# Performance work log

Hardware: AMD Instinct MI355X
Metric: run time of the kernel (lower is better)

## Reference

```python
import jax, jax.numpy as jnp
import numpy as np

MAX_RADIUS = 4.0
N_BASIS = 10
MUL = 8                    # output_size -> '8x0e' multiplicity
OUT_MULS = (16, 8, 4)      # irreps_output = 16x0e + 8x1o + 4x2e
L_DIMS = (1, 3, 5)
N_NODES = 10000
N_EDGES = 131072
N_GRAPHS = 64
WEIGHT_NUMEL = MUL * MUL * sum(OUT_MULS)  # 1792


def _silu(x):
    return x * jax.nn.sigmoid(x)


def _sph_harm(u):
    # e3nn real spherical harmonics lmax=2, normalize=True, 'component' normalization
    x, y, z = u[:, 0], u[:, 1], u[:, 2]
    s3, s5, s15 = 3.0 ** 0.5, 5.0 ** 0.5, 15.0 ** 0.5
    sh0 = jnp.ones_like(x)[:, None]
    sh1 = jnp.stack([s3 * x, s3 * y, s3 * z], -1)
    sh2 = jnp.stack([s15 * x * z, s15 * x * y,
                     s5 * (y * y - 0.5 * (x * x + z * z)),
                     s15 * y * z, 0.5 * s15 * (z * z - x * x)], -1)
    return sh0, sh1, sh2


def _soft_one_hot(x):
    # e3nn soft_one_hot_linspace, basis='gaussian', cutoff=True
    values = jnp.linspace(0.0, MAX_RADIUS, N_BASIS + 2)[1:-1]
    step = MAX_RADIUS / (N_BASIS + 1)
    diff = (x[:, None] - values) / step
    return jnp.exp(-diff * diff) / 1.12


def setup_inputs() -> dict:
    key = jax.random.key(0)
    ks = jax.random.split(key, 16)
    return {
        "pos": jax.random.normal(ks[0], (N_NODES, 3), jnp.float32) * 2.0,
        "A": jax.random.randint(ks[1], (N_NODES,), 0, 10),
        "batch": jnp.sort(jax.random.randint(ks[2], (N_NODES,), 0, N_GRAPHS)),
        "edge_src": jax.random.randint(ks[3], (N_EDGES,), 0, N_NODES),
        "edge_dst": jax.random.randint(ks[4], (N_EDGES,), 0, N_NODES),
        "edge_shifts": jax.random.normal(ks[5], (N_EDGES, 3), jnp.float32) * 0.1,
        "cell": jax.random.normal(ks[6], (N_GRAPHS, 3, 3), jnp.float32),
        "embed_table": jax.random.normal(ks[7], (10, 16), jnp.float32),
        "fit_W1": jax.random.normal(ks[8], (16, 64), jnp.float32) * (2.0 / 16) ** 0.5,
        "fit_b1": jnp.zeros((64,), jnp.float32),
        "fit_W2": jax.random.normal(ks[9], (64, 32), jnp.float32) * (2.0 / 64) ** 0.5,
        "fit_b2": jnp.zeros((32,), jnp.float32),
        "fit_W3": jax.random.normal(ks[10], (32, MUL), jnp.float32) * (2.0 / 32) ** 0.5,
        "fit_b3": jnp.zeros((MUL,), jnp.float32),
        "fc_W1": jax.random.normal(ks[11], (N_BASIS, 64), jnp.float32),
        "fc_W2": jax.random.normal(ks[12], (64, 64), jnp.float32),
        "fc_W3": jax.random.normal(ks[13], (64, 64), jnp.float32),
        "fc_W4": jax.random.normal(ks[14], (64, WEIGHT_NUMEL), jnp.float32),
    }


def reference(pos, A, batch, edge_src, edge_dst, edge_shifts, cell,
              embed_table, fit_W1, fit_b1, fit_W2, fit_b2, fit_W3, fit_b3,
              fc_W1, fc_W2, fc_W3, fc_W4):
    # --- edge vectors with periodic shifts ---
    shift_vecs = jnp.einsum('ni,nij->nj', edge_shifts, cell[batch[edge_src]])
    edge_vec = pos[edge_dst] - pos[edge_src] + shift_vecs      # [E,3]
    edge_length = jnp.linalg.norm(edge_vec, axis=1)            # [E]
    unit = edge_vec / jnp.maximum(edge_length, 1e-9)[:, None]

    # --- per-node scalar features: embedding -> MLP (MainNet2) ---
    h = embed_table[A]
    h = _silu(h @ fit_W1 + fit_b1)
    h = _silu(h @ fit_W2 + fit_b2)
    Ai = h @ fit_W3 + fit_b3                                   # [N,8]

    sh0, sh1, sh2 = _sph_harm(unit)                            # [E,1],[E,3],[E,5]

    # --- radial MLP (e3nn FullyConnectedNet: silu, 1/sqrt(fan_in) weight scaling) ---
    emb = _soft_one_hot(edge_length) * (N_BASIS ** 0.5)
    w = _silu(emb @ fc_W1 / N_BASIS ** 0.5)
    w = _silu(w @ fc_W2 / 8.0)
    w = _silu(w @ fc_W3 / 8.0)
    w = w @ fc_W4 / 8.0                                        # [E,1792]

    Ai_src = Ai[edge_src]                                      # [E,8]
    Ai_dst = Ai[edge_dst]                                      # [E,8]

    # FullTensorProduct(8x0e, sh) is the outer product f_in[e,u,m] = Ai_src[e,u]*sh_l[e,m];
    # FullyConnectedTensorProduct with scalar irreps_in2 reduces per l-channel to a
    # weighted contraction with path normalization 1/sqrt(mul1*mul2) = 1/8.
    blocks, off = [], 0
    for mul_out, dim, sh_l in zip(OUT_MULS, L_DIMS, (sh0, sh1, sh2)):
        n = MUL * MUL * mul_out
        Wl = w[:, off:off + n].reshape(-1, MUL, MUL, mul_out)
        off += n
        blk = jnp.einsum('eu,em,ev,euvw->ewm', Ai_src, sh_l, Ai_dst, Wl) / MUL
        blocks.append(blk.reshape(-1, mul_out * dim))
    edge_features = jnp.concatenate(blocks, -1)                # [E,60]

    # --- scatter-mean aggregation to destination nodes ---
    n_nodes = pos.shape[0]
    counts = jax.ops.segment_sum(jnp.ones((edge_dst.shape[0],), jnp.float32),
                                 edge_dst, num_segments=n_nodes)
    out = jax.ops.segment_sum(edge_features, edge_dst, num_segments=n_nodes)
    return out / jnp.maximum(counts, 1.0)[:, None]             # [N,60]
```

## Files before the change

kernel.cpp:

```cpp
#include <hip/hip_runtime.h>
#include <hip/hip_bf16.h>
#include <math.h>

#define NN 10000
#define NE 131072

typedef __attribute__((ext_vector_type(8))) short short8;
typedef __attribute__((ext_vector_type(4))) float f32x4;

__device__ __forceinline__ float silu_f(float x) {
    return x / (1.0f + __expf(-x));
}

__device__ __forceinline__ unsigned short f2bf(float f) {
    unsigned int u = __float_as_uint(f);
    u += 0x7FFFu + ((u >> 16) & 1u);
    return (unsigned short)(u >> 16);
}

__device__ __forceinline__ unsigned int pk_bf16(float lo, float hi) {
    __hip_bfloat162 h = __float22bfloat162_rn(float2{lo, hi});
    return *reinterpret_cast<unsigned int*>(&h);
}

__global__ __launch_bounds__(256)
void prep_kernel(const int* __restrict__ A,
                 const int* __restrict__ edst,
                 const float* __restrict__ emb_tab,
                 const float* __restrict__ W1, const float* __restrict__ b1,
                 const float* __restrict__ W2, const float* __restrict__ b2,
                 const float* __restrict__ W3, const float* __restrict__ b3,
                 const float* __restrict__ fcW1,
                 const float* __restrict__ fcW2,
                 const float* __restrict__ fcW3,
                 const float* __restrict__ fcW4,
                 int* __restrict__ hist,
                 int* __restrict__ rank,
                 float* __restrict__ outg,
                 float* __restrict__ Ai,
                 unsigned short* __restrict__ Wg,
                 unsigned short* __restrict__ Bg)
{
    const int blk = blockIdx.x;
    const int tid = threadIdx.x;

    if (blk < 40) {
        int nd = blk * 256 + tid;
        if (nd >= NN) return;
        int a = A[nd];
        float h[16];
#pragma unroll
        for (int i = 0; i < 16; ++i) h[i] = emb_tab[a * 16 + i];
        float h1[64];
#pragma unroll
        for (int j = 0; j < 64; ++j) h1[j] = b1[j];
#pragma unroll
        for (int i = 0; i < 16; ++i) {
            float hv = h[i];
#pragma unroll
            for (int j = 0; j < 64; ++j) h1[j] += hv * W1[i * 64 + j];
        }
#pragma unroll
        for (int j = 0; j < 64; ++j) h1[j] = silu_f(h1[j]);
        float h2[32];
#pragma unroll
        for (int j = 0; j < 32; ++j) h2[j] = b2[j];
#pragma unroll
        for (int i = 0; i < 64; ++i) {
            float hv = h1[i];
#pragma unroll
            for (int j = 0; j < 32; ++j) h2[j] += hv * W2[i * 32 + j];
        }
#pragma unroll
        for (int j = 0; j < 32; ++j) h2[j] = silu_f(h2[j]);
#pragma unroll
        for (int j = 0; j < 8; ++j) {
            float s = b3[j];
#pragma unroll
            for (int i = 0; i < 32; ++i) s += h2[i] * W3[i * 8 + j];
            Ai[nd * 8 + j] = s;
        }
    } else if (blk < 80) {
        int i = (blk - 40) * 256 + tid;
        int j    = i & 7;
        int lane = (i >> 3) & 63;
        int f    = i >> 9;
        int q = lane >> 4, n = lane & 15;
        int L, kf, nt;
        if (f < 4)       { L = 1; kf = 0;             nt = f; }
        else if (f < 12) { L = 2; kf = (f - 4) >> 2;  nt = (f - 4) & 3; }
        else             { L = 3; kf = (f - 12) >> 2; nt = (f - 12) & 3; }
        int k = kf * 32 + q * 8 + j;
        int col = nt * 16 + n;
        float v = 0.0f;
        if (L == 1)      { if (k < 10) v = fcW1[k * 64 + col]; }
        else if (L == 2) v = fcW2[k * 64 + col];
        else             v = fcW3[k * 64 + col];
        Wg[i] = f2bf(v);
    } else if (blk < 592) {
        int linear = (blk - 80) * 256 + tid;
        rank[linear] = atomicAdd(&hist[edst[linear]], 1);
        if (linear < 114688) {
            int k = linear / 1792;
            int t = linear - k * 1792;
            int uv, wc;
            if (t < 1024)      { uv = t >> 4;            wc = t & 15; }
            else if (t < 1536) { int r = t - 1024; uv = r >> 3; wc = 16 + (r & 7); }
            else               { int r = t - 1536; uv = r >> 2; wc = 24 + (r & 3); }
            int h  = uv >> 5;
            int q  = (uv >> 3) & 3;
            int j  = uv & 7;
            int nt = wc >> 4;
            int n  = wc & 15;
            int i  = (k << 11) | (h << 10) | (nt << 9) | (((q << 4) | n) << 3) | j;
            Bg[i] = f2bf(fcW4[linear]);
        } else {
            int z  = linear - 114688;
            int k  = z >> 8;
            int r  = z & 255;
            int uv = r >> 2;
            int c2 = z & 3;
            int h  = uv >> 5;
            int q  = (uv >> 3) & 3;
            int j  = uv & 7;
            int i  = (k << 11) | (h << 10) | (1 << 9) | (((q << 4) | (12 + c2)) << 3) | j;
            Bg[i] = 0;
        }
    } else {
        int t = (blk - 592) * 256 + tid;
        float4 z = float4{0.f, 0.f, 0.f, 0.f};
        for (int r = t; r < 150000; r += 25600)
            ((float4*)outg)[r] = z;
    }
}

__global__ __launch_bounds__(256)
void scanrank_kernel(const int* __restrict__ edst,
                     const int* __restrict__ hist,
                     const int* __restrict__ rank,
                     int* __restrict__ sortidx)
{
    __shared__ int offs[NN];
    __shared__ int part[256];
    const int tid = threadIdx.x;

    int loc[40];
    int s = 0;
    if (tid < 250) {
        const int4* h4 = (const int4*)(hist) + tid * 10;
#pragma unroll
        for (int v = 0; v < 10; ++v) {
            int4 x = h4[v];
            loc[v * 4 + 0] = x.x; loc[v * 4 + 1] = x.y;
            loc[v * 4 + 2] = x.z; loc[v * 4 + 3] = x.w;
            s += x.x + x.y + x.z + x.w;
        }
    } else {
#pragma unroll
        for (int r = 0; r < 40; ++r) loc[r] = 0;
    }
    part[tid] = s;
    __syncthreads();
#pragma unroll
    for (int off = 1; off < 256; off <<= 1) {
        int v = (tid >= off) ? part[tid - off] : 0;
        __syncthreads();
        part[tid] += v;
        __syncthreads();
    }
    if (tid < 250) {
        int run = part[tid] - s;
        int base = tid * 40;
#pragma unroll
        for (int r = 0; r < 40; ++r) { offs[base + r] = run; run += loc[r]; }
    }
    __syncthreads();

    int e = blockIdx.x * 256 + tid;
    int d = edst[e];
    sortidx[offs[d] + rank[e]] = e;
}

__global__ __launch_bounds__(256, 2)
void edge_fused_kernel(const float* __restrict__ pos,
                       const int* __restrict__ batch,
                       const int* __restrict__ esrc,
                       const int* __restrict__ edst,
                       const float* __restrict__ shifts,
                       const float* __restrict__ cell,
                       const unsigned short* __restrict__ Wg,
                       const unsigned short* __restrict__ Bg,
                       const int* __restrict__ sortidx,
                       const float* __restrict__ Ai,
                       const int* __restrict__ hist,
                       float* __restrict__ out_g)
{
    __shared__ __align__(16) unsigned short actb[4][64 * 68];
    __shared__ int   sdb[256];
    __shared__ __align__(16) float shb[4][64 * 8];

    const int tid  = threadIdx.x;
    const int wave = tid >> 6;
    const int lane = tid & 63;
    const int q    = lane >> 4;
    const int n    = lane & 15;
    const int i    = blockIdx.x * 256 + wave * 64 + lane;

    unsigned short* actw = actb[wave];

    int e = sortidx[i];
    int s = esrc[e], d = edst[e];
    sdb[wave * 64 + lane] = s | (d << 16);
    int b = batch[s];
    const float* C = cell + b * 9;
    float sx = shifts[e * 3 + 0], sy = shifts[e * 3 + 1], sz = shifts[e * 3 + 2];
    float vx = pos[d * 3 + 0] - pos[s * 3 + 0] + sx * C[0] + sy * C[3] + sz * C[6];
    float vy = pos[d * 3 + 1] - pos[s * 3 + 1] + sx * C[1] + sy * C[4] + sz * C[7];
    float vz = pos[d * 3 + 2] - pos[s * 3 + 2] + sx * C[2] + sy * C[5] + sz * C[8];
    float len = sqrtf(vx * vx + vy * vy + vz * vz);
    float inv = 1.0f / fmaxf(len, 1e-9f);
    float ux = vx * inv, uy = vy * inv, uz = vz * inv;
    {
        const float s3c  = 1.7320508075688772f;
        const float s5c  = 2.2360679774997896f;
        const float s15c = 3.872983346207417f;
        float* shw = shb[wave];
        *(float4*)&shw[lane * 8]     = float4{s3c * ux, s3c * uy, s3c * uz,
                                              s15c * ux * uz};
        *(float4*)&shw[lane * 8 + 4] = float4{s15c * ux * uy,
                                              s5c * (uy * uy - 0.5f * (ux * ux + uz * uz)),
                                              s15c * uy * uz,
                                              0.5f * s15c * (uz * uz - ux * ux)};
    }

    float embv[10];
    float base = len * 2.75f;
#pragma unroll
    for (int ii = 0; ii < 10; ++ii) {
        float ddv = base - (float)(ii + 1);
        embv[ii] = __expf(-ddv * ddv) * (1.0f / 1.12f);
    }
    {
        unsigned int u0 = pk_bf16(embv[0], embv[1]);
        unsigned int u1 = pk_bf16(embv[2], embv[3]);
        unsigned int u2 = pk_bf16(embv[4], embv[5]);
        unsigned int u3 = pk_bf16(embv[6], embv[7]);
        unsigned int u4 = pk_bf16(embv[8], embv[9]);
        uint2* arow = (uint2*)&actw[lane * 68];
        arow[0] = uint2{u0, u1};
        arow[1] = uint2{u2, u3};
        arow[2] = uint2{u4, 0u};
        arow[3] = uint2{0u, 0u};
        arow[4] = uint2{0u, 0u};
        arow[5] = uint2{0u, 0u};
        arow[6] = uint2{0u, 0u};
        arow[7] = uint2{0u, 0u};
    }

    union AF { unsigned int u[4]; short8 s8; };
    const f32x4 Z4 = (f32x4){0.f, 0.f, 0.f, 0.f};

    auto loadA = [&](int t, int kf) -> AF {
        const unsigned short* ap = &actw[(t * 16 + n) * 68 + kf * 32 + q * 8];
        uint2 a = *(const uint2*)ap;
        uint2 c = *(const uint2*)(ap + 4);
        AF f; f.u[0] = a.x; f.u[1] = a.y; f.u[2] = c.x; f.u[3] = c.y;
        return f;
    };
    auto loadW = [&](int f) -> short8 {
        return *(const short8*)&Wg[(f * 64 + lane) * 8];
    };

    {
        AF A1[4];
#pragma unroll
        for (int t = 0; t < 4; ++t) A1[t] = loadA(t, 0);
#pragma unroll
        for (int nt = 0; nt < 4; ++nt) {
            short8 W0 = loadW(nt);
            f32x4 Cc[4];
#pragma unroll
            for (int t = 0; t < 4; ++t)
                Cc[t] = __builtin_amdgcn_mfma_f32_16x16x32_bf16(A1[t].s8, W0, Z4, 0, 0, 0);
#pragma unroll
            for (int t = 0; t < 4; ++t)
#pragma unroll
                for (int r = 0; r < 4; ++r)
                    actw[(t * 16 + q * 4 + r) * 68 + nt * 16 + n] = f2bf(silu_f(Cc[t][r]));
        }
    }

    {
        AF A2[4][2];
#pragma unroll
        for (int t = 0; t < 4; ++t)
#pragma unroll
            for (int kf = 0; kf < 2; ++kf) A2[t][kf] = loadA(t, kf);
#pragma unroll
        for (int nt = 0; nt < 4; ++nt) {
            short8 Wk0 = loadW(4 + nt);
            short8 Wk1 = loadW(8 + nt);
            f32x4 Cc[4];
#pragma unroll
            for (int t = 0; t < 4; ++t) {
                Cc[t] = __builtin_amdgcn_mfma_f32_16x16x32_bf16(A2[t][0].s8, Wk0, Z4, 0, 0, 0);
                Cc[t] = __builtin_amdgcn_mfma_f32_16x16x32_bf16(A2[t][1].s8, Wk1, Cc[t], 0, 0, 0);
            }
#pragma unroll
            for (int t = 0; t < 4; ++t)
#pragma unroll
                for (int r = 0; r < 4; ++r)
                    actw[(t * 16 + q * 4 + r) * 68 + nt * 16 + n] = f2bf(silu_f(Cc[t][r] * 0.125f));
        }
    }

    {
        AF A3[4][2];
#pragma unroll
        for (int t = 0; t < 4; ++t)
#pragma unroll
            for (int kf = 0; kf < 2; ++kf) A3[t][kf] = loadA(t, kf);
#pragma unroll
        for (int nt = 0; nt < 4; ++nt) {
            short8 Wk0 = loadW(12 + nt);
            short8 Wk1 = loadW(16 + nt);
            f32x4 Cc[4];
#pragma unroll
            for (int t = 0; t < 4; ++t) {
                Cc[t] = __builtin_amdgcn_mfma_f32_16x16x32_bf16(A3[t][0].s8, Wk0, Z4, 0, 0, 0);
                Cc[t] = __builtin_amdgcn_mfma_f32_16x16x32_bf16(A3[t][1].s8, Wk1, Cc[t], 0, 0, 0);
            }
#pragma unroll
            for (int t = 0; t < 4; ++t)
#pragma unroll
                for (int r = 0; r < 4; ++r)
                    actw[(nt * 16 + n) * 68 + t * 16 + q * 4 + r] = f2bf(silu_f(Cc[t][r] * 0.125f));
        }
    }

    AF P[4][2];
#pragma unroll
    for (int t = 0; t < 4; ++t) {
        int eL = wave * 64 + t * 16 + n;
        int sd = sdb[eL];
        int ss  = sd & 0xFFFF;
        int dd2 = sd >> 16;
        float As0 = Ai[ss * 8 + q];
        float As1 = Ai[ss * 8 + 4 + q];
        float4 d0 = *(const float4*)&Ai[dd2 * 8];
        float4 d1 = *(const float4*)&Ai[dd2 * 8 + 4];
        float Ad[8] = {d0.x, d0.y, d0.z, d0.w, d1.x, d1.y, d1.z, d1.w};
#pragma unroll
        for (int h = 0; h < 2; ++h) {
            float s0 = h ? As1 : As0;
            P[t][h].u[0] = pk_bf16(s0 * Ad[0], s0 * Ad[1]);
            P[t][h].u[1] = pk_bf16(s0 * Ad[2], s0 * Ad[3]);
            P[t][h].u[2] = pk_bf16(s0 * Ad[4], s0 * Ad[5]);
            P[t][h].u[3] = pk_bf16(s0 * Ad[6], s0 * Ad[7]);
        }
    }

    f32x4 out[4][2];
#pragma unroll
    for (int t = 0; t < 4; ++t)
#pragma unroll
        for (int nt = 0; nt < 2; ++nt)
            out[t][nt] = (f32x4){0.f, 0.f, 0.f, 0.f};

    const unsigned char* BgB = (const unsigned char*)Bg;
#pragma unroll 2
    for (int c = 0; c < 32; ++c) {
#pragma unroll
        for (int kk = 0; kk < 2; ++kk) {
            int k = c * 2 + kk;
            short8 Bf[2][2];
#pragma unroll
            for (int h = 0; h < 2; ++h)
#pragma unroll
                for (int nt = 0; nt < 2; ++nt)
                    Bf[h][nt] = *(const short8*)(BgB +
                        (((size_t)((c * 8 + kk * 4 + h * 2 + nt) * 64 + lane)) << 4));
#pragma unroll
            for (int t = 0; t < 4; ++t) {
                uint2 v = *(const uint2*)&actw[k * 68 + t * 16 + q * 4];
                float w0 = __uint_as_float(v.x << 16);
                float w1 = __uint_as_float(v.x & 0xFFFF0000u);
                float w2 = __uint_as_float(v.y << 16);
                float w3 = __uint_as_float(v.y & 0xFFFF0000u);
#pragma unroll
                for (int nt = 0; nt < 2; ++nt) {
                    f32x4 Q = __builtin_amdgcn_mfma_f32_16x16x32_bf16(
                        P[t][0].s8, Bf[0][nt], Z4, 0, 0, 0);
                    Q = __builtin_amdgcn_mfma_f32_16x16x32_bf16(
                        P[t][1].s8, Bf[1][nt], Q, 0, 0, 0);
                    out[t][nt][0] += w0 * Q[0];
                    out[t][nt][1] += w1 * Q[1];
                    out[t][nt][2] += w2 * Q[2];
                    out[t][nt][3] += w3 * Q[3];
                }
            }
        }
    }

    float* featL = (float*)actw;
#pragma unroll
    for (int t = 0; t < 4; ++t) {
#pragma unroll
        for (int r = 0; r < 4; ++r) {
            int row = t * 16 + q * 4 + r;
            featL[row * 33 + n]      = out[t][0][r];
            featL[row * 33 + 16 + n] = out[t][1][r];
        }
    }

    if (lane < 60) {
        int j = lane;
        int cc, sidx = 0;
        bool is0 = (j < 16);
        if (j < 16)      { cc = j; }
        else if (j < 40) { cc = 16 + (j - 16) / 3; sidx = (j - 16) % 3; }
        else             { cc = 24 + (j - 40) / 5; sidx = 3 + (j - 40) % 5; }

        const float* shw = shb[wave];
        int cur_d = sdb[wave * 64] >> 16;
        float acc = 0.f;
        for (int e2 = 0; e2 < 64; ++e2) {
            int d_e = sdb[wave * 64 + e2] >> 16;
            if (d_e != cur_d) {
                int cnt = hist[cur_d];
                atomicAdd(&out_g[cur_d * 60 + j], acc * (1.0f / 64.0f) / (float)cnt);
                acc = 0.f;
                cur_d = d_e;
            }
            float f  = featL[e2 * 33 + cc];
            float sh = shw[e2 * 8 + sidx];
            if (is0) sh = 1.0f;
            acc += f * sh;
        }
        int cnt = hist[cur_d];
        atomicAdd(&out_g[cur_d * 60 + j], acc * (1.0f / 64.0f) / (float)cnt);
    }
}

extern "C" void kernel_launch(void* const* d_in, const int* in_sizes, int n_in,
                              void* d_out, int out_size, void* d_ws, size_t ws_size,
                              hipStream_t stream)
{
    const float* pos     = (const float*)d_in[0];
    const int*   A       = (const int*)d_in[1];
    const int*   batch   = (const int*)d_in[2];
    const int*   esrc    = (const int*)d_in[3];
    const int*   edst    = (const int*)d_in[4];
    const float* shifts  = (const float*)d_in[5];
    const float* cell    = (const float*)d_in[6];
    const float* emb_tab = (const float*)d_in[7];
    const float* fitW1   = (const float*)d_in[8];
    const float* fitb1   = (const float*)d_in[9];
    const float* fitW2   = (const float*)d_in[10];
    const float* fitb2   = (const float*)d_in[11];
    const float* fitW3   = (const float*)d_in[12];
    const float* fitb3   = (const float*)d_in[13];
    const float* fcW1    = (const float*)d_in[14];
    const float* fcW2    = (const float*)d_in[15];
    const float* fcW3    = (const float*)d_in[16];
    const float* fcW4    = (const float*)d_in[17];

    float* out = (float*)d_out;

    char* W = (char*)d_ws;
    float* Ai      = (float*)W;  W += (size_t)NN * 8 * 4;
    int* sortidx   = (int*)W;    W += (size_t)NE * 4;
    int* rank      = (int*)W;    W += (size_t)NE * 4;
    int* hist      = (int*)W;    W += (size_t)NN * 4;
    unsigned short* Bg = (unsigned short*)W; W += (size_t)131072 * 2;
    unsigned short* Wg = (unsigned short*)W; W += (size_t)10240 * 2;

    hipMemsetAsync(hist, 0, (size_t)NN * 4, stream);

    prep_kernel<<<692, 256, 0, stream>>>(
        A, edst, emb_tab, fitW1, fitb1, fitW2, fitb2, fitW3, fitb3,
        fcW1, fcW2, fcW3, fcW4, hist, rank, out, Ai, Wg, Bg);

    scanrank_kernel<<<NE / 256, 256, 0, stream>>>(edst, hist, rank, sortidx);

    edge_fused_kernel<<<NE / 256, 256, 0, stream>>>(
        pos, batch, esrc, edst, shifts, cell, Wg, Bg,
        sortidx, Ai, hist, out);
}
```

Measured before the change: 196.2 us.

## Halve edges per wave to 32, drop shared buffers, raise occupancy

Each wave now processes 32 edges instead of 64, and the grid doubles. The src/dst indices and unit vectors stay in registers and are broadcast with shuffles, so the sdb and shb shared buffers are gone and the spherical harmonics are recomputed in the aggregation loop. Launch bounds rise to 4 blocks per CU, aiming to cut register and LDS pressure and improve latency hiding. In exchange, half the lanes sit idle during edge geometry, more weight loads are repeated across waves, destination runs are shorter so atomics increase, and the per-lane branches in the aggregation loop add work.

```diff
diff --git a/kernel.cpp b/kernel.cpp
--- a/kernel.cpp
+++ b/kernel.cpp
@@ -181,7 +181,7 @@
     sortidx[offs[d] + rank[e]] = e;
 }
 
-__global__ __launch_bounds__(256, 2)
+__global__ __launch_bounds__(256, 4)
 void edge_fused_kernel(const float* __restrict__ pos,
                        const int* __restrict__ batch,
                        const int* __restrict__ esrc,
@@ -195,58 +195,46 @@
                        const int* __restrict__ hist,
                        float* __restrict__ out_g)
 {
-    __shared__ __align__(16) unsigned short actb[4][64 * 68];
-    __shared__ int   sdb[256];
-    __shared__ __align__(16) float shb[4][64 * 8];
+    __shared__ __align__(16) unsigned short actb[4][2304];
 
     const int tid  = threadIdx.x;
     const int wave = tid >> 6;
     const int lane = tid & 63;
     const int q    = lane >> 4;
     const int n    = lane & 15;
-    const int i    = blockIdx.x * 256 + wave * 64 + lane;
 
     unsigned short* actw = actb[wave];
 
-    int e = sortidx[i];
-    int s = esrc[e], d = edst[e];
-    sdb[wave * 64 + lane] = s | (d << 16);
-    int b = batch[s];
-    const float* C = cell + b * 9;
-    float sx = shifts[e * 3 + 0], sy = shifts[e * 3 + 1], sz = shifts[e * 3 + 2];
-    float vx = pos[d * 3 + 0] - pos[s * 3 + 0] + sx * C[0] + sy * C[3] + sz * C[6];
-    float vy = pos[d * 3 + 1] - pos[s * 3 + 1] + sx * C[1] + sy * C[4] + sz * C[7];
-    float vz = pos[d * 3 + 2] - pos[s * 3 + 2] + sx * C[2] + sy * C[5] + sz * C[8];
-    float len = sqrtf(vx * vx + vy * vy + vz * vz);
-    float inv = 1.0f / fmaxf(len, 1e-9f);
-    float ux = vx * inv, uy = vy * inv, uz = vz * inv;
-    {
-        const float s3c  = 1.7320508075688772f;
-        const float s5c  = 2.2360679774997896f;
-        const float s15c = 3.872983346207417f;
-        float* shw = shb[wave];
-        *(float4*)&shw[lane * 8]     = float4{s3c * ux, s3c * uy, s3c * uz,
-                                              s15c * ux * uz};
-        *(float4*)&shw[lane * 8 + 4] = float4{s15c * ux * uy,
-                                              s5c * (uy * uy - 0.5f * (ux * ux + uz * uz)),
-                                              s15c * uy * uz,
-                                              0.5f * s15c * (uz * uz - ux * ux)};
-    }
-
-    float embv[10];
-    float base = len * 2.75f;
-#pragma unroll
-    for (int ii = 0; ii < 10; ++ii) {
-        float ddv = base - (float)(ii + 1);
-        embv[ii] = __expf(-ddv * ddv) * (1.0f / 1.12f);
-    }
-    {
+    int   sd_self = 0;
+    float uxr = 0.f, uyr = 0.f, uzr = 0.f;
+    if (lane < 32) {
+        int i = blockIdx.x * 128 + wave * 32 + lane;
+        int e = sortidx[i];
+        int s = esrc[e], d = edst[e];
+        sd_self = s | (d << 16);
+        int b = batch[s];
+        const float* C = cell + b * 9;
+        float sx = shifts[e * 3 + 0], sy = shifts[e * 3 + 1], sz = shifts[e * 3 + 2];
+        float vx = pos[d * 3 + 0] - pos[s * 3 + 0] + sx * C[0] + sy * C[3] + sz * C[6];
+        float vy = pos[d * 3 + 1] - pos[s * 3 + 1] + sx * C[1] + sy * C[4] + sz * C[7];
+        float vz = pos[d * 3 + 2] - pos[s * 3 + 2] + sx * C[2] + sy * C[5] + sz * C[8];
+        float len = sqrtf(vx * vx + vy * vy + vz * vz);
+        float inv = 1.0f / fmaxf(len, 1e-9f);
+        uxr = vx * inv; uyr = vy * inv; uzr = vz * inv;
+
+        float embv[10];
+        float base = len * 2.75f;
+#pragma unroll
+        for (int ii = 0; ii < 10; ++ii) {
+            float ddv = base - (float)(ii + 1);
+            embv[ii] = __expf(-ddv * ddv) * (1.0f / 1.12f);
+        }
         unsigned int u0 = pk_bf16(embv[0], embv[1]);
         unsigned int u1 = pk_bf16(embv[2], embv[3]);
         unsigned int u2 = pk_bf16(embv[4], embv[5]);
         unsigned int u3 = pk_bf16(embv[6], embv[7]);
         unsigned int u4 = pk_bf16(embv[8], embv[9]);
-        uint2* arow = (uint2*)&actw[lane * 68];
+        uint2* arow = (uint2*)&actw[lane * 72];
         arow[0] = uint2{u0, u1};
         arow[1] = uint2{u2, u3};
         arow[2] = uint2{u4, 0u};
@@ -261,7 +249,7 @@
     const f32x4 Z4 = (f32x4){0.f, 0.f, 0.f, 0.f};
 
     auto loadA = [&](int t, int kf) -> AF {
-        const unsigned short* ap = &actw[(t * 16 + n) * 68 + kf * 32 + q * 8];
+        const unsigned short* ap = &actw[(t * 16 + n) * 72 + kf * 32 + q * 8];
         uint2 a = *(const uint2*)ap;
         uint2 c = *(const uint2*)(ap + 4);
         AF f; f.u[0] = a.x; f.u[1] = a.y; f.u[2] = c.x; f.u[3] = c.y;
@@ -272,77 +260,77 @@
     };
 
     {
-        AF A1[4];
-#pragma unroll
-        for (int t = 0; t < 4; ++t) A1[t] = loadA(t, 0);
+        AF A1[2];
+#pragma unroll
+        for (int t = 0; t < 2; ++t) A1[t] = loadA(t, 0);
 #pragma unroll
         for (int nt = 0; nt < 4; ++nt) {
             short8 W0 = loadW(nt);
-            f32x4 Cc[4];
-#pragma unroll
-            for (int t = 0; t < 4; ++t)
+            f32x4 Cc[2];
+#pragma unroll
+            for (int t = 0; t < 2; ++t)
                 Cc[t] = __builtin_amdgcn_mfma_f32_16x16x32_bf16(A1[t].s8, W0, Z4, 0, 0, 0);
 #pragma unroll
-            for (int t = 0; t < 4; ++t)
+            for (int t = 0; t < 2; ++t)
 #pragma unroll
                 for (int r = 0; r < 4; ++r)
-                    actw[(t * 16 + q * 4 + r) * 68 + nt * 16 + n] = f2bf(silu_f(Cc[t][r]));
+                    actw[(t * 16 + q * 4 + r) * 72 + nt * 16 + n] = f2bf(silu_f(Cc[t][r]));
         }
     }
 
     {
-        AF A2[4][2];
-#pragma unroll
-        for (int t = 0; t < 4; ++t)
+        AF A2[2][2];
+#pragma unroll
+        for (int t = 0; t < 2; ++t)
 #pragma unroll
             for (int kf = 0; kf < 2; ++kf) A2[t][kf] = loadA(t, kf);
 #pragma unroll
         for (int nt = 0; nt < 4; ++nt) {
             short8 Wk0 = loadW(4 + nt);
             short8 Wk1 = loadW(8 + nt);
-            f32x4 Cc[4];
-#pragma unroll
-            for (int t = 0; t < 4; ++t) {
+            f32x4 Cc[2];
+#pragma unroll
+            for (int t = 0; t < 2; ++t) {
                 Cc[t] = __builtin_amdgcn_mfma_f32_16x16x32_bf16(A2[t][0].s8, Wk0, Z4, 0, 0, 0);
                 Cc[t] = __builtin_amdgcn_mfma_f32_16x16x32_bf16(A2[t][1].s8, Wk1, Cc[t], 0, 0, 0);
             }
 #pragma unroll
-            for (int t = 0; t < 4; ++t)
+            for (int t = 0; t < 2; ++t)
 #pragma unroll
                 for (int r = 0; r < 4; ++r)
-                    actw[(t * 16 + q * 4 + r) * 68 + nt * 16 + n] = f2bf(silu_f(Cc[t][r] * 0.125f));
+                    actw[(t * 16 + q * 4 + r) * 72 + nt * 16 + n] = f2bf(silu_f(Cc[t][r] * 0.125f));
         }
     }
 
     {
-        AF A3[4][2];
-#pragma unroll
-        for (int t = 0; t < 4; ++t)
+        AF A3[2][2];
+#pragma unroll
+        for (int t = 0; t < 2; ++t)
 #pragma unroll
             for (int kf = 0; kf < 2; ++kf) A3[t][kf] = loadA(t, kf);
 #pragma unroll
         for (int nt = 0; nt < 4; ++nt) {
             short8 Wk0 = loadW(12 + nt);
             short8 Wk1 = loadW(16 + nt);
-            f32x4 Cc[4];
-#pragma unroll
-            for (int t = 0; t < 4; ++t) {
+            f32x4 Cc[2];
+#pragma unroll
+            for (int t = 0; t < 2; ++t) {
                 Cc[t] = __builtin_amdgcn_mfma_f32_16x16x32_bf16(A3[t][0].s8, Wk0, Z4, 0, 0, 0);
                 Cc[t] = __builtin_amdgcn_mfma_f32_16x16x32_bf16(A3[t][1].s8, Wk1, Cc[t], 0, 0, 0);
             }
 #pragma unroll
-            for (int t = 0; t < 4; ++t)
+            for (int t = 0; t < 2; ++t)
 #pragma unroll
                 for (int r = 0; r < 4; ++r)
-                    actw[(nt * 16 + n) * 68 + t * 16 + q * 4 + r] = f2bf(silu_f(Cc[t][r] * 0.125f));
-        }
-    }
-
-    AF P[4][2];
-#pragma unroll
-    for (int t = 0; t < 4; ++t) {
-        int eL = wave * 64 + t * 16 + n;
-        int sd = sdb[eL];
+                    actw[(nt * 16 + n) * 36 + t * 16 + q * 4 + r] = f2bf(silu_f(Cc[t][r] * 0.125f));
+        }
+    }
+
+    AF P[2][2];
+#pragma unroll
+    for (int t = 0; t < 2; ++t) {
+        int eL = t * 16 + n;
+        int sd = __shfl(sd_self, eL);
         int ss  = sd & 0xFFFF;
         int dd2 = sd >> 16;
         float As0 = Ai[ss * 8 + q];
@@ -360,9 +348,9 @@
         }
     }
 
-    f32x4 out[4][2];
-#pragma unroll
-    for (int t = 0; t < 4; ++t)
+    f32x4 out[2][2];
+#pragma unroll
+    for (int t = 0; t < 2; ++t)
 #pragma unroll
         for (int nt = 0; nt < 2; ++nt)
             out[t][nt] = (f32x4){0.f, 0.f, 0.f, 0.f};
@@ -381,8 +369,8 @@
                     Bf[h][nt] = *(const short8*)(BgB +
                         (((size_t)((c * 8 + kk * 4 + h * 2 + nt) * 64 + lane)) << 4));
 #pragma unroll
-            for (int t = 0; t < 4; ++t) {
-                uint2 v = *(const uint2*)&actw[k * 68 + t * 16 + q * 4];
+            for (int t = 0; t < 2; ++t) {
+                uint2 v = *(const uint2*)&actw[k * 36 + t * 16 + q * 4];
                 float w0 = __uint_as_float(v.x << 16);
                 float w1 = __uint_as_float(v.x & 0xFFFF0000u);
                 float w2 = __uint_as_float(v.y << 16);
@@ -404,7 +392,7 @@
 
     float* featL = (float*)actw;
 #pragma unroll
-    for (int t = 0; t < 4; ++t) {
+    for (int t = 0; t < 2; ++t) {
 #pragma unroll
         for (int r = 0; r < 4; ++r) {
             int row = t * 16 + q * 4 + r;
@@ -413,32 +401,49 @@
         }
     }
 
-    if (lane < 60) {
+    {
+        const float s3c  = 1.7320508075688772f;
+        const float s5c  = 2.2360679774997896f;
+        const float s15c = 3.872983346207417f;
         int j = lane;
-        int cc, sidx = 0;
-        bool is0 = (j < 16);
-        if (j < 16)      { cc = j; }
-        else if (j < 40) { cc = 16 + (j - 16) / 3; sidx = (j - 16) % 3; }
-        else             { cc = 24 + (j - 40) / 5; sidx = 3 + (j - 40) % 5; }
-
-        const float* shw = shb[wave];
-        int cur_d = sdb[wave * 64] >> 16;
+        int cc = 0, mode = 0, m = 0;
+        if (j < 16)      { cc = j; mode = 0; }
+        else if (j < 40) { int w = (j - 16) / 3; m = (j - 16) % 3; cc = 16 + w; mode = 1; }
+        else if (j < 60) { int w = (j - 40) / 5; m = (j - 40) % 5; cc = 24 + w; mode = 2; }
+
+        int cur_d = __shfl(sd_self, 0) >> 16;
         float acc = 0.f;
-        for (int e2 = 0; e2 < 64; ++e2) {
-            int d_e = sdb[wave * 64 + e2] >> 16;
+        for (int e2 = 0; e2 < 32; ++e2) {
+            int   sdv = __shfl(sd_self, e2);
+            float uxe = __shfl(uxr, e2);
+            float uye = __shfl(uyr, e2);
+            float uze = __shfl(uzr, e2);
+            int d_e = sdv >> 16;
             if (d_e != cur_d) {
-                int cnt = hist[cur_d];
-                atomicAdd(&out_g[cur_d * 60 + j], acc * (1.0f / 64.0f) / (float)cnt);
+                if (j < 60) {
+                    int cnt = hist[cur_d];
+                    atomicAdd(&out_g[cur_d * 60 + j], acc * (1.0f / 64.0f) / (float)cnt);
+                }
                 acc = 0.f;
                 cur_d = d_e;
             }
-            float f  = featL[e2 * 33 + cc];
-            float sh = shw[e2 * 8 + sidx];
-            if (is0) sh = 1.0f;
+            float f = featL[e2 * 33 + cc];
+            float sh = 1.f;
+            if (mode == 1) {
+                sh = s3c * (m == 0 ? uxe : (m == 1 ? uye : uze));
+            } else if (mode == 2) {
+                if (m == 0)      sh = s15c * uxe * uze;
+                else if (m == 1) sh = s15c * uxe * uye;
+                else if (m == 2) sh = s5c * (uye * uye - 0.5f * (uxe * uxe + uze * uze));
+                else if (m == 3) sh = s15c * uye * uze;
+                else             sh = 0.5f * s15c * (uze * uze - uxe * uxe);
+            }
             acc += f * sh;
         }
-        int cnt = hist[cur_d];
-        atomicAdd(&out_g[cur_d * 60 + j], acc * (1.0f / 64.0f) / (float)cnt);
+        if (j < 60) {
+            int cnt = hist[cur_d];
+            atomicAdd(&out_g[cur_d * 60 + j], acc * (1.0f / 64.0f) / (float)cnt);
+        }
     }
 }
 
@@ -483,7 +488,7 @@
 
     scanrank_kernel<<<NE / 256, 256, 0, stream>>>(edst, hist, rank, sortidx);
 
-    edge_fused_kernel<<<NE / 256, 256, 0, stream>>>(
+    edge_fused_kernel<<<NE / 128, 256, 0, stream>>>(
         pos, batch, esrc, edst, shifts, cell, Wg, Bg,
         sortidx, Ai, hist, out);
 }
```

Result: slower. 213.7 us (+8.9%).
